# Optimization experiments

Measured on AMD Instinct MI355X. Metric: run time of the kernel, lower is better.

Reference implementation:

```python
import jax, jax.numpy as jnp
import numpy as np

B, MENU, N, M = 4096, 256, 8, 16


def setup_inputs() -> dict:
    key = jax.random.key(0)
    k1, k2, k3, k4 = jax.random.split(key, 4)
    input_bids = jax.random.uniform(k1, (B, N, M), dtype=jnp.float32)
    allocs = jax.random.uniform(k2, (B, MENU, N, M), dtype=jnp.float32)
    # bidder weights must be strictly positive (divided by in payments)
    w = jax.random.uniform(k3, (B, N), dtype=jnp.float32, minval=0.5, maxval=1.5)
    b = jax.random.normal(k4, (B, MENU), dtype=jnp.float32)
    softmax_temp = jnp.asarray(100.0, dtype=jnp.float32)
    return {"input_bids": input_bids, "allocs": allocs, "w": w, "b": b,
            "softmax_temp": softmax_temp}


def reference(input_bids, allocs, w, b, softmax_temp):
    Bsz, n, m = input_bids.shape
    # append the "null" menu entry (zero allocation, zero boost)
    allocs = jnp.concatenate([allocs, jnp.zeros((Bsz, 1, n, m), allocs.dtype)], axis=1)  # B,S,n,m
    b = jnp.concatenate([b, jnp.zeros((Bsz, 1), b.dtype)], axis=1)                        # B,S

    # utility of each agent under each menu entry
    util = jnp.einsum('bsnm,bnm->bsn', allocs, input_bids)        # B,S,n
    per_agent_welfare = w[:, None, :] * util                      # B,S,n
    total_welfare = per_agent_welfare.sum(-1)                     # B,S

    alloc_choice = jax.nn.softmax((total_welfare + b) * softmax_temp, axis=-1)  # B,S
    item_allocation = jnp.einsum('bs,bsnm->bnm', alloc_choice, allocs)          # B,n,m
    chosen_welfare = jnp.einsum('bsn,bs->bn', per_agent_welfare, alloc_choice)  # B,n

    # leave-one-out (VCG-style) payments, vectorized over the removed agent i
    mask = 1.0 - jnp.eye(n, dtype=per_agent_welfare.dtype)        # n,n; row i zeros agent i
    removed_welfare = per_agent_welfare[None] * mask[:, None, None, :]  # i,B,S,n
    total_removed = removed_welfare.sum(-1)                       # i,B,S
    removed_choice = jax.nn.softmax((total_removed + b[None]) * softmax_temp, axis=-1)  # i,B,S

    removed_chosen_sum = jnp.einsum('ibsn,ibs->ib', removed_welfare, removed_choice)  # i,B
    masked_chosen_sum = jnp.einsum('bn,in->ib', chosen_welfare, mask)                 # i,B
    removed_b = jnp.einsum('ibs,bs->ib', removed_choice, b)                           # i,B
    alloc_b = jnp.einsum('bs,bs->b', alloc_choice, b)                                 # B

    payments = (removed_chosen_sum + removed_b - masked_chosen_sum - alloc_b[None]) / w.T  # n,B
    return alloc_choice, item_allocation, payments, allocs
```

## Files before the change

### kernel.cpp

```cpp
#include <hip/hip_runtime.h>

#define NAGENTS 8
#define NM 128
#define MENU 256
#define SFULL 257

typedef float f32x4 __attribute__((ext_vector_type(4)));

#define BAR() asm volatile("s_waitcnt lgkmcnt(0)\n\ts_barrier" ::: "memory")

__global__ __launch_bounds__(256, 8) void cama_kernel(
    const float* __restrict__ bids,
    const float* __restrict__ allocs,
    const float* __restrict__ wvec,
    const float* __restrict__ bvec,
    const float* __restrict__ tempp,
    float* __restrict__ out, int Bsz)
{
    __shared__ float lds_tot[MENU];
    __shared__ float lds_bb[MENU];
    __shared__ __align__(16) float4 lds_accs[4][32];
    __shared__ __align__(16) float4 lds_w1[4];
    __shared__ __align__(16) float4 lds_loo[4][8];
    __shared__ float lds_scw[4][8];
    __shared__ float lds_rcs[NAGENTS], lds_rb[NAGENTS], lds_cw[NAGENTS];
    __shared__ float lds_ab;
    __shared__ float2 lds_mzf;

    const int u = threadIdx.x;
    const int lane = u & 63;
    const int wave = u >> 6;
    const int c = u & 31;
    const int n = c >> 2;
    const int mq = u & 3;
    const int su = u >> 5;
    const size_t bb_ = (size_t)blockIdx.x;

    float* out_choice = out;
    float* out_item   = out + (size_t)Bsz * SFULL;
    float* out_pay    = out_item + (size_t)Bsz * NM;
    float* out_all    = out_pay + (size_t)NAGENTS * Bsz;
    f32x4* out_all4   = (f32x4*)out_all + bb_ * 8224;
    const f32x4* src4 = (const f32x4*)allocs + bb_ * 8192;

    const float temp = tempp[0];
    lds_bb[u] = bvec[bb_ * MENU + u];
    const float4 q4 = ((const float4*)(bids + bb_ * NM))[c];
    const float w_n = wvec[bb_ * NAGENTS + n];
    BAR();

    float M1 = -1e30f, Z1 = 0.f, Sab = 0.f, Scw = 0.f;
    float4 A = make_float4(0.f, 0.f, 0.f, 0.f);
    float M2 = -1e30f, Z2 = 0.f, S1 = 0.f, S2 = 0.f;

#pragma unroll 4
    for (int k = 0; k < 32; ++k) {
        const int idx = (k << 8) + u;
        f32x4 a4 = src4[idx];
        out_all4[idx] = a4;
        const int s = (k << 3) + su;
        const float bbs = lds_bb[s];
        float util = a4[0]*q4.x + a4[1]*q4.y + a4[2]*q4.z + a4[3]*q4.w;
        util += __shfl_xor(util, 1);
        util += __shfl_xor(util, 2);
        float pwv = w_n * util;
        float t = pwv;
        t += __shfl_xor(t, 4);
        t += __shfl_xor(t, 8);
        t += __shfl_xor(t, 16);
        if (c == 0) lds_tot[s] = t;
        float x = (t + bbs) * temp;
        float mn = fmaxf(M1, x);
        float sc = __expf(M1 - mn);
        float p  = __expf(x - mn);
        Z1  = Z1*sc + p;
        A.x = A.x*sc + p*a4[0];
        A.y = A.y*sc + p*a4[1];
        A.z = A.z*sc + p*a4[2];
        A.w = A.w*sc + p*a4[3];
        Sab = Sab*sc + p*bbs;
        Scw = Scw*sc + p*pwv;
        M1 = mn;
        float tr = t - pwv;
        float x2 = (tr + bbs) * temp;
        float mn2 = fmaxf(M2, x2);
        float sc2 = __expf(M2 - mn2);
        float p2  = __expf(x2 - mn2);
        Z2 = Z2*sc2 + p2;
        S1 = S1*sc2 + p2*tr;
        S2 = S2*sc2 + p2*bbs;
        M2 = mn2;
    }
    if (u < 32) {
        f32x4 z4 = {0.f, 0.f, 0.f, 0.f};
        out_all4[8192 + u] = z4;
    }

    {
        float Mo = __shfl_xor(M1, 32), Zo = __shfl_xor(Z1, 32);
        float Sabo = __shfl_xor(Sab, 32), Scwo = __shfl_xor(Scw, 32);
        float ax = __shfl_xor(A.x, 32), ay = __shfl_xor(A.y, 32);
        float az = __shfl_xor(A.z, 32), aw = __shfl_xor(A.w, 32);
        float mn = fmaxf(M1, Mo);
        float s0 = __expf(M1 - mn), s1 = __expf(Mo - mn);
        Z1  = Z1*s0  + Zo*s1;
        Sab = Sab*s0 + Sabo*s1;
        Scw = Scw*s0 + Scwo*s1;
        A.x = A.x*s0 + ax*s1;  A.y = A.y*s0 + ay*s1;
        A.z = A.z*s0 + az*s1;  A.w = A.w*s0 + aw*s1;
        M1 = mn;

        float Mo2 = __shfl_xor(M2, 32), Zo2 = __shfl_xor(Z2, 32);
        float S1o = __shfl_xor(S1, 32), S2o = __shfl_xor(S2, 32);
        float mn2 = fmaxf(M2, Mo2);
        float t0 = __expf(M2 - mn2), t1 = __expf(Mo2 - mn2);
        Z2 = Z2*t0 + Zo2*t1;
        S1 = S1*t0 + S1o*t1;
        S2 = S2*t0 + S2o*t1;
        M2 = mn2;

        if (lane < 32) {
            lds_accs[wave][c] = make_float4(A.x, A.y, A.z, A.w);
            if (c == 0) lds_w1[wave] = make_float4(M1, Z1, Sab, 0.f);
            if (mq == 0) {
                lds_scw[wave][n] = Scw;
                lds_loo[wave][n] = make_float4(M2, Z2, S1, S2);
            }
        }
    }
    BAR();

    if (u < 32) {
        float4 w1 = lds_w1[0];
        float Mm = w1.x, Zm = w1.y, Sabm = w1.z;
        float4 Am = lds_accs[0][u];
#pragma unroll
        for (int j = 1; j < 4; ++j) {
            float4 wj = lds_w1[j];
            float4 Aj = lds_accs[j][u];
            float mn = fmaxf(Mm, wj.x);
            float s0 = __expf(Mm - mn), s1 = __expf(wj.x - mn);
            Zm   = Zm*s0   + wj.y*s1;
            Sabm = Sabm*s0 + wj.z*s1;
            Am.x = Am.x*s0 + Aj.x*s1;  Am.y = Am.y*s0 + Aj.y*s1;
            Am.z = Am.z*s0 + Aj.z*s1;  Am.w = Am.w*s0 + Aj.w*s1;
            Mm = mn;
        }
        float M1f = fmaxf(Mm, 0.f);
        float s0 = __expf(Mm - M1f);
        float Z1f = Zm*s0 + __expf(-M1f);
        float inv = 1.f / Z1f;
        float sf = s0 * inv;
        ((float4*)(out_item + bb_ * NM))[u] =
            make_float4(Am.x*sf, Am.y*sf, Am.z*sf, Am.w*sf);
        if (u == 0) {
            lds_ab = Sabm * sf;
            lds_mzf = make_float2(M1f, inv);
        }
    } else if (u < 40) {
        const int i = u - 32;
        float4 L = lds_loo[0][i];
        float Mm = L.x, Zm = L.y, S1m = L.z, S2m = L.w;
#pragma unroll
        for (int j = 1; j < 4; ++j) {
            float4 Lj = lds_loo[j][i];
            float mn = fmaxf(Mm, Lj.x);
            float s0 = __expf(Mm - mn), s1 = __expf(Lj.x - mn);
            Zm  = Zm*s0  + Lj.y*s1;
            S1m = S1m*s0 + Lj.z*s1;
            S2m = S2m*s0 + Lj.w*s1;
            Mm = mn;
        }
        float M2f = fmaxf(Mm, 0.f);
        float s0 = __expf(Mm - M2f);
        float Z2f = Zm*s0 + __expf(-M2f);
        lds_rcs[i] = S1m*s0 / Z2f;
        lds_rb[i]  = S2m*s0 / Z2f;
    } else if (u < 48) {
        const int i = u - 40;
        float4 w1 = lds_w1[0];
        float Mm = w1.x, Zm = w1.y;
        float Sm = lds_scw[0][i];
#pragma unroll
        for (int j = 1; j < 4; ++j) {
            float4 wj = lds_w1[j];
            float mn = fmaxf(Mm, wj.x);
            float s0 = __expf(Mm - mn), s1 = __expf(wj.x - mn);
            Zm = Zm*s0 + wj.y*s1;
            Sm = Sm*s0 + lds_scw[j][i]*s1;
            Mm = mn;
        }
        float M1f = fmaxf(Mm, 0.f);
        float s0 = __expf(Mm - M1f);
        float Z1f = Zm*s0 + __expf(-M1f);
        lds_cw[i] = Sm*s0 / Z1f;
    }
    BAR();

    {
        float2 mzf = lds_mzf;
        float x = (lds_tot[u] + lds_bb[u]) * temp;
        out_choice[bb_ * SFULL + u] = __expf(x - mzf.x) * mzf.y;
        if (u == 0)
            out_choice[bb_ * SFULL + MENU] = __expf(-mzf.x) * mzf.y;
    }
    if (u < NAGENTS) {
        float ctot = 0.f;
#pragma unroll
        for (int k = 0; k < NAGENTS; ++k) ctot += lds_cw[k];
        float pay = (lds_rcs[u] + lds_rb[u] - (ctot - lds_cw[u]) - lds_ab)
                    / wvec[bb_ * NAGENTS + u];
        out_pay[(size_t)u * Bsz + bb_] = pay;
    }
}

extern "C" void kernel_launch(void* const* d_in, const int* in_sizes, int n_in,
                              void* d_out, int out_size, void* d_ws, size_t ws_size,
                              hipStream_t stream) {
    const float* bids   = (const float*)d_in[0];
    const float* allocs = (const float*)d_in[1];
    const float* wvec   = (const float*)d_in[2];
    const float* bvec   = (const float*)d_in[3];
    const float* tempp  = (const float*)d_in[4];
    float* out = (float*)d_out;
    const int Bsz = in_sizes[0] / NM;
    cama_kernel<<<Bsz, 256, 0, stream>>>(bids, allocs, wvec, bvec, tempp,
                                         out, Bsz);
}
```

Before: 233.7 us.

## Process two batch elements per block with cross-element prefetch

```diff
diff --git a/kernel.cpp b/kernel.cpp
--- a/kernel.cpp
+++ b/kernel.cpp
@@ -17,8 +17,8 @@
     const float* __restrict__ tempp,
     float* __restrict__ out, int Bsz)
 {
-    __shared__ float lds_tot[MENU];
-    __shared__ float lds_bb[MENU];
+    __shared__ float lds_tot[2][MENU];
+    __shared__ float lds_bb[2][MENU];
     __shared__ __align__(16) float4 lds_accs[4][32];
     __shared__ __align__(16) float4 lds_w1[4];
     __shared__ __align__(16) float4 lds_loo[4][8];
@@ -34,183 +34,212 @@
     const int n = c >> 2;
     const int mq = u & 3;
     const int su = u >> 5;
-    const size_t bb_ = (size_t)blockIdx.x;
+    const size_t a0 = (size_t)blockIdx.x * 2;
 
     float* out_choice = out;
     float* out_item   = out + (size_t)Bsz * SFULL;
     float* out_pay    = out_item + (size_t)Bsz * NM;
     float* out_all    = out_pay + (size_t)NAGENTS * Bsz;
-    f32x4* out_all4   = (f32x4*)out_all + bb_ * 8224;
-    const f32x4* src4 = (const f32x4*)allocs + bb_ * 8192;
 
     const float temp = tempp[0];
-    lds_bb[u] = bvec[bb_ * MENU + u];
-    const float4 q4 = ((const float4*)(bids + bb_ * NM))[c];
-    const float w_n = wvec[bb_ * NAGENTS + n];
-    BAR();
-
-    float M1 = -1e30f, Z1 = 0.f, Sab = 0.f, Scw = 0.f;
-    float4 A = make_float4(0.f, 0.f, 0.f, 0.f);
-    float M2 = -1e30f, Z2 = 0.f, S1 = 0.f, S2 = 0.f;
-
-#pragma unroll 4
-    for (int k = 0; k < 32; ++k) {
-        const int idx = (k << 8) + u;
-        f32x4 a4 = src4[idx];
-        out_all4[idx] = a4;
-        const int s = (k << 3) + su;
-        const float bbs = lds_bb[s];
-        float util = a4[0]*q4.x + a4[1]*q4.y + a4[2]*q4.z + a4[3]*q4.w;
-        util += __shfl_xor(util, 1);
-        util += __shfl_xor(util, 2);
-        float pwv = w_n * util;
-        float t = pwv;
-        t += __shfl_xor(t, 4);
-        t += __shfl_xor(t, 8);
-        t += __shfl_xor(t, 16);
-        if (c == 0) lds_tot[s] = t;
-        float x = (t + bbs) * temp;
-        float mn = fmaxf(M1, x);
-        float sc = __expf(M1 - mn);
-        float p  = __expf(x - mn);
-        Z1  = Z1*sc + p;
-        A.x = A.x*sc + p*a4[0];
-        A.y = A.y*sc + p*a4[1];
-        A.z = A.z*sc + p*a4[2];
-        A.w = A.w*sc + p*a4[3];
-        Sab = Sab*sc + p*bbs;
-        Scw = Scw*sc + p*pwv;
-        M1 = mn;
-        float tr = t - pwv;
-        float x2 = (tr + bbs) * temp;
-        float mn2 = fmaxf(M2, x2);
-        float sc2 = __expf(M2 - mn2);
-        float p2  = __expf(x2 - mn2);
-        Z2 = Z2*sc2 + p2;
-        S1 = S1*sc2 + p2*tr;
-        S2 = S2*sc2 + p2*bbs;
-        M2 = mn2;
-    }
-    if (u < 32) {
-        f32x4 z4 = {0.f, 0.f, 0.f, 0.f};
-        out_all4[8192 + u] = z4;
-    }
-
+
+    lds_bb[0][u] = bvec[a0 * MENU + u];
+    float4 q4 = ((const float4*)(bids + a0 * NM))[c];
+    float w_n = wvec[a0 * NAGENTS + n];
+    f32x4 pf0, pf1;
     {
-        float Mo = __shfl_xor(M1, 32), Zo = __shfl_xor(Z1, 32);
-        float Sabo = __shfl_xor(Sab, 32), Scwo = __shfl_xor(Scw, 32);
-        float ax = __shfl_xor(A.x, 32), ay = __shfl_xor(A.y, 32);
-        float az = __shfl_xor(A.z, 32), aw = __shfl_xor(A.w, 32);
-        float mn = fmaxf(M1, Mo);
-        float s0 = __expf(M1 - mn), s1 = __expf(Mo - mn);
-        Z1  = Z1*s0  + Zo*s1;
-        Sab = Sab*s0 + Sabo*s1;
-        Scw = Scw*s0 + Scwo*s1;
-        A.x = A.x*s0 + ax*s1;  A.y = A.y*s0 + ay*s1;
-        A.z = A.z*s0 + az*s1;  A.w = A.w*s0 + aw*s1;
-        M1 = mn;
-
-        float Mo2 = __shfl_xor(M2, 32), Zo2 = __shfl_xor(Z2, 32);
-        float S1o = __shfl_xor(S1, 32), S2o = __shfl_xor(S2, 32);
-        float mn2 = fmaxf(M2, Mo2);
-        float t0 = __expf(M2 - mn2), t1 = __expf(Mo2 - mn2);
-        Z2 = Z2*t0 + Zo2*t1;
-        S1 = S1*t0 + S1o*t1;
-        S2 = S2*t0 + S2o*t1;
-        M2 = mn2;
-
-        if (lane < 32) {
-            lds_accs[wave][c] = make_float4(A.x, A.y, A.z, A.w);
-            if (c == 0) lds_w1[wave] = make_float4(M1, Z1, Sab, 0.f);
-            if (mq == 0) {
-                lds_scw[wave][n] = Scw;
-                lds_loo[wave][n] = make_float4(M2, Z2, S1, S2);
-            }
-        }
+        const f32x4* s4 = (const f32x4*)allocs + a0 * 8192;
+        pf0 = s4[u];
+        pf1 = s4[256 + u];
     }
     BAR();
 
-    if (u < 32) {
-        float4 w1 = lds_w1[0];
-        float Mm = w1.x, Zm = w1.y, Sabm = w1.z;
-        float4 Am = lds_accs[0][u];
-#pragma unroll
-        for (int j = 1; j < 4; ++j) {
-            float4 wj = lds_w1[j];
-            float4 Aj = lds_accs[j][u];
-            float mn = fmaxf(Mm, wj.x);
-            float s0 = __expf(Mm - mn), s1 = __expf(wj.x - mn);
-            Zm   = Zm*s0   + wj.y*s1;
-            Sabm = Sabm*s0 + wj.z*s1;
-            Am.x = Am.x*s0 + Aj.x*s1;  Am.y = Am.y*s0 + Aj.y*s1;
-            Am.z = Am.z*s0 + Aj.z*s1;  Am.w = Am.w*s0 + Aj.w*s1;
-            Mm = mn;
-        }
-        float M1f = fmaxf(Mm, 0.f);
-        float s0 = __expf(Mm - M1f);
-        float Z1f = Zm*s0 + __expf(-M1f);
-        float inv = 1.f / Z1f;
-        float sf = s0 * inv;
-        ((float4*)(out_item + bb_ * NM))[u] =
-            make_float4(Am.x*sf, Am.y*sf, Am.z*sf, Am.w*sf);
-        if (u == 0) {
-            lds_ab = Sabm * sf;
-            lds_mzf = make_float2(M1f, inv);
-        }
-    } else if (u < 40) {
-        const int i = u - 32;
-        float4 L = lds_loo[0][i];
-        float Mm = L.x, Zm = L.y, S1m = L.z, S2m = L.w;
-#pragma unroll
-        for (int j = 1; j < 4; ++j) {
-            float4 Lj = lds_loo[j][i];
-            float mn = fmaxf(Mm, Lj.x);
-            float s0 = __expf(Mm - mn), s1 = __expf(Lj.x - mn);
-            Zm  = Zm*s0  + Lj.y*s1;
-            S1m = S1m*s0 + Lj.z*s1;
-            S2m = S2m*s0 + Lj.w*s1;
-            Mm = mn;
-        }
-        float M2f = fmaxf(Mm, 0.f);
-        float s0 = __expf(Mm - M2f);
-        float Z2f = Zm*s0 + __expf(-M2f);
-        lds_rcs[i] = S1m*s0 / Z2f;
-        lds_rb[i]  = S2m*s0 / Z2f;
-    } else if (u < 48) {
-        const int i = u - 40;
-        float4 w1 = lds_w1[0];
-        float Mm = w1.x, Zm = w1.y;
-        float Sm = lds_scw[0][i];
-#pragma unroll
-        for (int j = 1; j < 4; ++j) {
-            float4 wj = lds_w1[j];
-            float mn = fmaxf(Mm, wj.x);
-            float s0 = __expf(Mm - mn), s1 = __expf(wj.x - mn);
-            Zm = Zm*s0 + wj.y*s1;
-            Sm = Sm*s0 + lds_scw[j][i]*s1;
-            Mm = mn;
-        }
-        float M1f = fmaxf(Mm, 0.f);
-        float s0 = __expf(Mm - M1f);
-        float Z1f = Zm*s0 + __expf(-M1f);
-        lds_cw[i] = Sm*s0 / Z1f;
-    }
-    BAR();
-
-    {
-        float2 mzf = lds_mzf;
-        float x = (lds_tot[u] + lds_bb[u]) * temp;
-        out_choice[bb_ * SFULL + u] = __expf(x - mzf.x) * mzf.y;
-        if (u == 0)
-            out_choice[bb_ * SFULL + MENU] = __expf(-mzf.x) * mzf.y;
-    }
-    if (u < NAGENTS) {
-        float ctot = 0.f;
-#pragma unroll
-        for (int k = 0; k < NAGENTS; ++k) ctot += lds_cw[k];
-        float pay = (lds_rcs[u] + lds_rb[u] - (ctot - lds_cw[u]) - lds_ab)
-                    / wvec[bb_ * NAGENTS + u];
-        out_pay[(size_t)u * Bsz + bb_] = pay;
+    float4 q4n = q4; float wn_n = w_n, rbbn = 0.f;
+
+    for (int h = 0; h < 2; ++h) {
+        const size_t aa = a0 + h;
+        const f32x4* src4 = (const f32x4*)allocs + aa * 8192;
+        f32x4* oa4 = (f32x4*)out_all + aa * 8224;
+
+        float M1 = -1e30f, Z1 = 0.f, Sab = 0.f, Scw = 0.f;
+        float4 A = make_float4(0.f, 0.f, 0.f, 0.f);
+        float M2 = -1e30f, Z2 = 0.f, S1 = 0.f, S2 = 0.f;
+
+        auto body = [&](f32x4 a4, int k) {
+            oa4[(k << 8) + u] = a4;
+            const int s = (k << 3) + su;
+            const float bbs = lds_bb[h][s];
+            float util = a4[0]*q4.x + a4[1]*q4.y + a4[2]*q4.z + a4[3]*q4.w;
+            util += __shfl_xor(util, 1);
+            util += __shfl_xor(util, 2);
+            float pwv = w_n * util;
+            float t = pwv;
+            t += __shfl_xor(t, 4);
+            t += __shfl_xor(t, 8);
+            t += __shfl_xor(t, 16);
+            if (c == 0) lds_tot[h][s] = t;
+            float x = (t + bbs) * temp;
+            float mn = fmaxf(M1, x);
+            float sc = __expf(M1 - mn);
+            float p  = __expf(x - mn);
+            Z1  = Z1*sc + p;
+            A.x = A.x*sc + p*a4[0];
+            A.y = A.y*sc + p*a4[1];
+            A.z = A.z*sc + p*a4[2];
+            A.w = A.w*sc + p*a4[3];
+            Sab = Sab*sc + p*bbs;
+            Scw = Scw*sc + p*pwv;
+            M1 = mn;
+            float tr = t - pwv;
+            float x2 = (tr + bbs) * temp;
+            float mn2 = fmaxf(M2, x2);
+            float sc2 = __expf(M2 - mn2);
+            float p2  = __expf(x2 - mn2);
+            Z2 = Z2*sc2 + p2;
+            S1 = S1*sc2 + p2*tr;
+            S2 = S2*sc2 + p2*bbs;
+            M2 = mn2;
+        };
+
+        body(pf0, 0);
+        body(pf1, 1);
+#pragma unroll 5
+        for (int k = 2; k < 32; ++k) {
+            f32x4 a4 = src4[(k << 8) + u];
+            body(a4, k);
+        }
+        if (u < 32) {
+            f32x4 z4 = {0.f, 0.f, 0.f, 0.f};
+            oa4[8192 + u] = z4;
+        }
+        if (h == 0) {
+            const f32x4* s4n = (const f32x4*)allocs + (aa + 1) * 8192;
+            pf0 = s4n[u];
+            pf1 = s4n[256 + u];
+            rbbn = bvec[(aa + 1) * MENU + u];
+            q4n = ((const float4*)(bids + (aa + 1) * NM))[c];
+            wn_n = wvec[(aa + 1) * NAGENTS + n];
+        }
+
+        {
+            float Mo = __shfl_xor(M1, 32), Zo = __shfl_xor(Z1, 32);
+            float Sabo = __shfl_xor(Sab, 32), Scwo = __shfl_xor(Scw, 32);
+            float ax = __shfl_xor(A.x, 32), ay = __shfl_xor(A.y, 32);
+            float az = __shfl_xor(A.z, 32), aw = __shfl_xor(A.w, 32);
+            float mn = fmaxf(M1, Mo);
+            float s0 = __expf(M1 - mn), s1 = __expf(Mo - mn);
+            Z1  = Z1*s0  + Zo*s1;
+            Sab = Sab*s0 + Sabo*s1;
+            Scw = Scw*s0 + Scwo*s1;
+            A.x = A.x*s0 + ax*s1;  A.y = A.y*s0 + ay*s1;
+            A.z = A.z*s0 + az*s1;  A.w = A.w*s0 + aw*s1;
+            M1 = mn;
+
+            float Mo2 = __shfl_xor(M2, 32), Zo2 = __shfl_xor(Z2, 32);
+            float S1o = __shfl_xor(S1, 32), S2o = __shfl_xor(S2, 32);
+            float mn2 = fmaxf(M2, Mo2);
+            float t0 = __expf(M2 - mn2), t1 = __expf(Mo2 - mn2);
+            Z2 = Z2*t0 + Zo2*t1;
+            S1 = S1*t0 + S1o*t1;
+            S2 = S2*t0 + S2o*t1;
+            M2 = mn2;
+
+            if (lane < 32) {
+                lds_accs[wave][c] = make_float4(A.x, A.y, A.z, A.w);
+                if (c == 0) lds_w1[wave] = make_float4(M1, Z1, Sab, 0.f);
+                if (mq == 0) {
+                    lds_scw[wave][n] = Scw;
+                    lds_loo[wave][n] = make_float4(M2, Z2, S1, S2);
+                }
+            }
+        }
+        BAR();
+
+        if (h == 0) lds_bb[1][u] = rbbn;
+
+        if (u < 32) {
+            float4 w1 = lds_w1[0];
+            float Mm = w1.x, Zm = w1.y, Sabm = w1.z;
+            float4 Am = lds_accs[0][u];
+#pragma unroll
+            for (int j = 1; j < 4; ++j) {
+                float4 wj = lds_w1[j];
+                float4 Aj = lds_accs[j][u];
+                float mn = fmaxf(Mm, wj.x);
+                float s0 = __expf(Mm - mn), s1 = __expf(wj.x - mn);
+                Zm   = Zm*s0   + wj.y*s1;
+                Sabm = Sabm*s0 + wj.z*s1;
+                Am.x = Am.x*s0 + Aj.x*s1;  Am.y = Am.y*s0 + Aj.y*s1;
+                Am.z = Am.z*s0 + Aj.z*s1;  Am.w = Am.w*s0 + Aj.w*s1;
+                Mm = mn;
+            }
+            float M1f = fmaxf(Mm, 0.f);
+            float s0 = __expf(Mm - M1f);
+            float Z1f = Zm*s0 + __expf(-M1f);
+            float inv = 1.f / Z1f;
+            float sf = s0 * inv;
+            ((float4*)(out_item + aa * NM))[u] =
+                make_float4(Am.x*sf, Am.y*sf, Am.z*sf, Am.w*sf);
+            if (u == 0) {
+                lds_ab = Sabm * sf;
+                lds_mzf = make_float2(M1f, inv);
+            }
+        } else if (u < 40) {
+            const int i = u - 32;
+            float4 L = lds_loo[0][i];
+            float Mm = L.x, Zm = L.y, S1m = L.z, S2m = L.w;
+#pragma unroll
+            for (int j = 1; j < 4; ++j) {
+                float4 Lj = lds_loo[j][i];
+                float mn = fmaxf(Mm, Lj.x);
+                float s0 = __expf(Mm - mn), s1 = __expf(Lj.x - mn);
+                Zm  = Zm*s0  + Lj.y*s1;
+                S1m = S1m*s0 + Lj.z*s1;
+                S2m = S2m*s0 + Lj.w*s1;
+                Mm = mn;
+            }
+            float M2f = fmaxf(Mm, 0.f);
+            float s0 = __expf(Mm - M2f);
+            float Z2f = Zm*s0 + __expf(-M2f);
+            lds_rcs[i] = S1m*s0 / Z2f;
+            lds_rb[i]  = S2m*s0 / Z2f;
+        } else if (u < 48) {
+            const int i = u - 40;
+            float4 w1 = lds_w1[0];
+            float Mm = w1.x, Zm = w1.y;
+            float Sm = lds_scw[0][i];
+#pragma unroll
+            for (int j = 1; j < 4; ++j) {
+                float4 wj = lds_w1[j];
+                float mn = fmaxf(Mm, wj.x);
+                float s0 = __expf(Mm - mn), s1 = __expf(wj.x - mn);
+                Zm = Zm*s0 + wj.y*s1;
+                Sm = Sm*s0 + lds_scw[j][i]*s1;
+                Mm = mn;
+            }
+            float M1f = fmaxf(Mm, 0.f);
+            float s0 = __expf(Mm - M1f);
+            float Z1f = Zm*s0 + __expf(-M1f);
+            lds_cw[i] = Sm*s0 / Z1f;
+        }
+        BAR();
+
+        {
+            float2 mzf = lds_mzf;
+            float x = (lds_tot[h][u] + lds_bb[h][u]) * temp;
+            out_choice[aa * SFULL + u] = __expf(x - mzf.x) * mzf.y;
+            if (u == 0)
+                out_choice[aa * SFULL + MENU] = __expf(-mzf.x) * mzf.y;
+        }
+        if (u < NAGENTS) {
+            float ctot = 0.f;
+#pragma unroll
+            for (int k = 0; k < NAGENTS; ++k) ctot += lds_cw[k];
+            float pay = (lds_rcs[u] + lds_rb[u] - (ctot - lds_cw[u]) - lds_ab)
+                        / wvec[aa * NAGENTS + u];
+            out_pay[(size_t)u * Bsz + aa] = pay;
+        }
+        q4 = q4n; w_n = wn_n;
     }
 }
 
@@ -224,6 +253,6 @@
     const float* tempp  = (const float*)d_in[4];
     float* out = (float*)d_out;
     const int Bsz = in_sizes[0] / NM;
-    cama_kernel<<<Bsz, 256, 0, stream>>>(bids, allocs, wvec, bvec, tempp,
-                                         out, Bsz);
+    cama_kernel<<<Bsz / 2, 256, 0, stream>>>(bids, allocs, wvec, bvec, tempp,
+                                             out, Bsz);
 }
```

Measured after the change: 266.0 us. 13.8% more time.
